# Optimization experiments

Hardware: AMD Instinct MI355X
Metric: run time of the kernel (lower is better)

Reference implementation:

```python
import jax, jax.numpy as jnp
import numpy as np

MIN_VAR = 1e-4
B_SZ, T, X, U, A_DIM = 256, 256, 16, 8, 32


def setup_inputs() -> dict:
    key = jax.random.key(0)
    ks = jax.random.split(key, 8)
    return {
        "mean0": jax.random.normal(ks[0], (B_SZ, X), jnp.float32),
        "cov0": jnp.broadcast_to(jnp.eye(X, dtype=jnp.float32), (B_SZ, X, X)),
        "u": jax.random.normal(ks[1], (B_SZ, T, U), jnp.float32),
        "a": jax.random.normal(ks[2], (B_SZ, T, A_DIM), jnp.float32),
        "M": jnp.eye(X, dtype=jnp.float32),
        "N": jnp.eye(X, dtype=jnp.float32),
        "d": jax.random.normal(ks[3], (X,), jnp.float32),
        "B": jax.random.normal(ks[4], (X, U), jnp.float32),
        "C": jax.random.normal(ks[5], (A_DIM, X), jnp.float32),
        "nx": jax.random.normal(ks[6], (X,), jnp.float32),
        "na": jax.random.normal(ks[7], (A_DIM,), jnp.float32),
    }


def _compute_A(M, N, d):
    # A = U diag(sqrt(d)) Q diag(1/sqrt(1+d)) U^T, with Q, U sign-fixed QR factors
    dsp = jax.nn.softplus(d)
    Q, R = jnp.linalg.qr(M)
    Q = Q * jnp.sign(jnp.diagonal(R))[None, :]
    Uq, R2 = jnp.linalg.qr(N)
    Uq = Uq * jnp.sign(jnp.diagonal(R2))[None, :]
    return Uq @ (jnp.sqrt(dsp)[:, None] * Q) @ ((1.0 / jnp.sqrt(1.0 + dsp))[:, None] * Uq.T)


def reference(mean0, cov0, u, a, M, N, d, B, C, nx, na):
    A = _compute_A(M, N, d)
    Nx = jnp.diag(jax.nn.softplus(nx) + MIN_VAR)  # (x,x)
    Na = jnp.diag(jax.nn.softplus(na) + MIN_VAR)  # (a,a)

    def step(carry, inp):
        mean, cov = carry          # (b,x), (b,x,x)
        u_t, a_t = inp             # (b,u), (b,a)
        # dynamics update
        mean = mean @ A.T + u_t @ B.T
        cov = jnp.einsum('ij,bjk,lk->bil', A, cov, A) + Nx
        # measurement update
        S = jnp.einsum('ij,bjk,lk->bil', C, cov, C) + Na      # (b,a,a)
        K = jnp.einsum('bij,kj,bkl->bil', cov, C, jnp.linalg.pinv(S))  # (b,x,a)
        innov = a_t - mean @ C.T                              # (b,a)
        mean = mean + jnp.einsum('ba,bxa->bx', innov, K)
        cov = cov - jnp.einsum('bxa,ay,byk->bxk', K, C, cov)  # (I - K C) cov
        return (mean, cov), mean

    us = jnp.swapaxes(u, 0, 1)  # (T,b,u)
    as_ = jnp.swapaxes(a, 0, 1)  # (T,b,a)
    (_, _), means = jax.lax.scan(step, (mean0, cov0), (us, as_))
    return jnp.swapaxes(means, 0, 1)  # (b,T,x) filtered means
```

## Files before the change

### kernel.cpp

```cpp
#include <hip/hip_runtime.h>
#include <math.h>

#define TT 256
#define WARM 16
#define OFF_K    5632
#define OFF_MC   14336
#define OFF_NB   18688
#define OFF_P0   20864
#define OFF_PP   21120
#define OFF_WSEG 21376
#define OFF_BND  86912
#define NEED_WS_BYTES ((size_t)152448 * 4)

__device__ __forceinline__ float softplus(float v) {
    return fmaxf(v, 0.0f) + log1pf(expf(-fabsf(v)));
}

__device__ __forceinline__ void gj16(float (&aug)[8], const int i, const int gq) {
#pragma unroll
    for (int j = 0; j < 16; ++j) {
        float prow[8];
#pragma unroll
        for (int k = 0; k < 8; ++k) prow[k] = __shfl(aug[k], j + 16 * gq);
        const float pjj = __shfl(aug[j & 7], j + 16 * (j >> 3));
        const float cij = __shfl(aug[j & 7], i + 16 * (j >> 3));
        const float pivinv = 1.0f / pjj;
        const float f = cij * pivinv;
#pragma unroll
        for (int k = 0; k < 8; ++k)
            aug[k] = (i == j) ? prow[k] * pivinv : aug[k] - f * prow[k];
    }
}

#define LD_ROW16(Mt, r, row) do { \
    const float4 r0_ = *(const float4*)&Mt[r][0]; \
    const float4 r1_ = *(const float4*)&Mt[r][4]; \
    const float4 r2_ = *(const float4*)&Mt[r][8]; \
    const float4 r3_ = *(const float4*)&Mt[r][12]; \
    row[0]=r0_.x;  row[1]=r0_.y;  row[2]=r0_.z;  row[3]=r0_.w; \
    row[4]=r1_.x;  row[5]=r1_.y;  row[6]=r1_.z;  row[7]=r1_.w; \
    row[8]=r2_.x;  row[9]=r2_.y;  row[10]=r2_.z; row[11]=r2_.w; \
    row[12]=r3_.x; row[13]=r3_.y; row[14]=r3_.z; row[15]=r3_.w; } while (0)

__global__ __launch_bounds__(64) void chain_k(
    const float* __restrict__ Mm, const float* __restrict__ Nm,
    const float* __restrict__ dvec, const float* __restrict__ Bm,
    const float* __restrict__ Cm, const float* __restrict__ nx,
    const float* __restrict__ na, const float* __restrict__ cov0,
    float* __restrict__ wsK, float* __restrict__ wsM, float* __restrict__ wsN)
{
    __shared__ float qm[16][17], qn[16][17], T0s[16][17];
    __shared__ float sC[32][17], sW[16][33], sAm[16][17], sBm[16][9];
    __shared__ float sCA[32][17], sCB[32][9], sP[16][17], sK[16][33];
    __shared__ float spv[16], d2[16], sNai[32], sNxi[16];
    __shared__ __attribute__((aligned(16))) float mE[16][20];
    __shared__ __attribute__((aligned(16))) float mET[16][20];
    __shared__ __attribute__((aligned(16))) float mF[16][20];
    __shared__ __attribute__((aligned(16))) float mH[16][20];
    __shared__ __attribute__((aligned(16))) float mZ[16][20];
    __shared__ __attribute__((aligned(16))) float mT[16][20];
    __shared__ __attribute__((aligned(16))) float mT2[16][20];
    __shared__ __attribute__((aligned(16))) float mL[16][20];
    const int lane = threadIdx.x;
    const int t = blockIdx.x;
    const int n = t + 1;
    const int i = lane & 15, gq = lane >> 4;
    const int jj = gq << 2;

    for (int e = lane; e < 256; e += 64) { qm[e >> 4][e & 15] = Mm[e]; qn[e >> 4][e & 15] = Nm[e]; }
    for (int e = lane; e < 512; e += 64) sC[e >> 4][e & 15] = Cm[e];
    for (int e = lane; e < 128; e += 64) sBm[e >> 3][e & 7] = Bm[e];
    if (lane < 16) {
        float s = softplus(dvec[lane]);
        spv[lane] = sqrtf(s);
        d2[lane] = 1.0f / sqrtf(1.0f + s);
        sNxi[lane] = 1.0f / (softplus(nx[lane]) + 1e-4f);
    }
    if (lane < 32) sNai[lane] = 1.0f / (softplus(na[lane]) + 1e-4f);
    __syncthreads();

    {
        const int j0 = lane & 15;
        const int mi = lane >> 4;
        float (*Qs)[17] = (mi == 1) ? qn : qm;
        float col[16];
#pragma unroll
        for (int r = 0; r < 16; ++r) col[r] = Qs[r][j0];
        const int base = lane & 48;
#pragma unroll 1
        for (int j = 0; j < 16; ++j) {
            float qj[16];
#pragma unroll
            for (int r = 0; r < 16; ++r) qj[r] = __shfl(col[r], base + j);
            float nrm = 0.f;
#pragma unroll
            for (int r = 0; r < 16; ++r) nrm += qj[r] * qj[r];
            const float scal = 1.0f / sqrtf(nrm);
#pragma unroll
            for (int r = 0; r < 16; ++r) qj[r] *= scal;
            if (j0 == j) {
#pragma unroll
                for (int r = 0; r < 16; ++r) col[r] = qj[r];
            } else if (j0 > j) {
                float pr = 0.f;
#pragma unroll
                for (int r = 0; r < 16; ++r) pr += qj[r] * col[r];
#pragma unroll
                for (int r = 0; r < 16; ++r) col[r] -= pr * qj[r];
            }
        }
        __syncthreads();
        if (mi < 2) {
#pragma unroll
            for (int r = 0; r < 16; ++r) Qs[r][j0] = col[r];
        }
    }
    __syncthreads();

    for (int e = lane; e < 256; e += 64) {
        int ii = e >> 4, j = e & 15;
        float s = 0.f;
        for (int q = 0; q < 16; ++q) s += qm[ii][q] * d2[q] * qn[j][q];
        T0s[ii][j] = spv[ii] * s;
    }
    __syncthreads();
    for (int e = lane; e < 256; e += 64) {
        int ii = e >> 4, j = e & 15;
        float s = 0.f;
        for (int q = 0; q < 16; ++q) s += qn[ii][q] * T0s[q][j];
        sAm[ii][j] = s;
    }
    for (int e = lane; e < 512; e += 64) {
        int q = e >> 5, r = e & 31;
        sW[q][r] = sC[r][q] * sNai[r];
    }
    __syncthreads();
    for (int e = lane; e < 256; e += 64) {
        int ii = e >> 4, j = e & 15;
        float g = 0.f;
        for (int r = 0; r < 32; ++r) g += sC[r][ii] * sW[j][r];
        mF[ii][j] = g + ((ii == j) ? sNxi[ii] : 0.f);
        const float ev = sNxi[ii] * sAm[ii][j];
        mE[ii][j] = ev;
        mET[j][ii] = ev;
        float hsum = 0.f;
        for (int q = 0; q < 16; ++q) hsum += sAm[q][ii] * sNxi[q] * sAm[q][j];
        mH[ii][j] = hsum;
    }
    for (int e = lane; e < 512; e += 64) {
        int r = e >> 4, j = e & 15;
        float s = 0.f;
        for (int q = 0; q < 16; ++q) s += sC[r][q] * sAm[q][j];
        sCA[r][j] = s;
    }
    for (int e = lane; e < 256; e += 64) {
        int r = e >> 3, j = e & 7;
        float s = 0.f;
        for (int q = 0; q < 16; ++q) s += sC[r][q] * sBm[q][j];
        sCB[r][j] = s;
    }
    __syncthreads();

    float Er[16], ETr[16];
    LD_ROW16(mE, i, Er);
    LD_ROW16(mET, i, ETr);

    float aug[8];
#pragma unroll
    for (int k = 0; k < 8; ++k)
        aug[k] = (gq < 2) ? cov0[i * 16 + 8 * gq + k]
                          : ((8 * (gq - 2) + k == i) ? 1.f : 0.f);
    gj16(aug, i, gq);
    if (gq >= 2) {
        *(float4*)&mL[i][8 * (gq - 2)]     = make_float4(aug[0], aug[1], aug[2], aug[3]);
        *(float4*)&mL[i][8 * (gq - 2) + 4] = make_float4(aug[4], aug[5], aug[6], aug[7]);
    }
    __syncthreads();

#pragma unroll 1
    for (int m = 0; m < 5; ++m) {
        if ((n >> m) & 1) {
            if (gq < 2) {
                const float4 l0 = *(const float4*)&mL[i][8 * gq];
                const float4 l1 = *(const float4*)&mL[i][8 * gq + 4];
                const float4 h0 = *(const float4*)&mH[i][8 * gq];
                const float4 h1 = *(const float4*)&mH[i][8 * gq + 4];
                aug[0] = l0.x + h0.x; aug[1] = l0.y + h0.y;
                aug[2] = l0.z + h0.z; aug[3] = l0.w + h0.w;
                aug[4] = l1.x + h1.x; aug[5] = l1.y + h1.y;
                aug[6] = l1.z + h1.z; aug[7] = l1.w + h1.w;
            } else {
#pragma unroll
                for (int k = 0; k < 8; ++k) aug[k] = (8 * (gq - 2) + k == i) ? 1.f : 0.f;
            }
            gj16(aug, i, gq);
            if (gq >= 2) {
                *(float4*)&mZ[i][8 * (gq - 2)]     = make_float4(aug[0], aug[1], aug[2], aug[3]);
                *(float4*)&mZ[i][8 * (gq - 2) + 4] = make_float4(aug[4], aug[5], aug[6], aug[7]);
            }
            __syncthreads();
            {
                float4 zz[16];
#pragma unroll
                for (int q = 0; q < 16; ++q) zz[q] = *(const float4*)&mZ[q][jj];
                float4 tacc = make_float4(0.f, 0.f, 0.f, 0.f);
#pragma unroll
                for (int q = 0; q < 16; ++q) {
                    tacc.x += Er[q] * zz[q].x; tacc.y += Er[q] * zz[q].y;
                    tacc.z += Er[q] * zz[q].z; tacc.w += Er[q] * zz[q].w;
                }
                *(float4*)&mT[i][jj] = tacc;
            }
            __syncthreads();
            {
                float Tr[16];
                LD_ROW16(mT, i, Tr);
                float4 et[16];
#pragma unroll
                for (int q = 0; q < 16; ++q) et[q] = *(const float4*)&mET[q][jj];
                float4 l = *(const float4*)&mF[i][jj];
#pragma unroll
                for (int q = 0; q < 16; ++q) {
                    l.x -= Tr[q] * et[q].x; l.y -= Tr[q] * et[q].y;
                    l.z -= Tr[q] * et[q].z; l.w -= Tr[q] * et[q].w;
                }
                __syncthreads();
                *(float4*)&mL[i][jj] = l;
            }
            __syncthreads();
        }
        if (m < 4 && (n >> (m + 1)) != 0) {
            if (gq < 2) {
                const float4 f0 = *(const float4*)&mF[i][8 * gq];
                const float4 f1 = *(const float4*)&mF[i][8 * gq + 4];
                const float4 h0 = *(const float4*)&mH[i][8 * gq];
                const float4 h1 = *(const float4*)&mH[i][8 * gq + 4];
                aug[0] = f0.x + h0.x; aug[1] = f0.y + h0.y;
                aug[2] = f0.z + h0.z; aug[3] = f0.w + h0.w;
                aug[4] = f1.x + h1.x; aug[5] = f1.y + h1.y;
                aug[6] = f1.z + h1.z; aug[7] = f1.w + h1.w;
            } else {
#pragma unroll
                for (int k = 0; k < 8; ++k) aug[k] = (8 * (gq - 2) + k == i) ? 1.f : 0.f;
            }
            gj16(aug, i, gq);
            if (gq >= 2) {
                *(float4*)&mZ[i][8 * (gq - 2)]     = make_float4(aug[0], aug[1], aug[2], aug[3]);
                *(float4*)&mZ[i][8 * (gq - 2) + 4] = make_float4(aug[4], aug[5], aug[6], aug[7]);
            }
            __syncthreads();
            {
                float4 zz[16];
#pragma unroll
                for (int q = 0; q < 16; ++q) zz[q] = *(const float4*)&mZ[q][jj];
                float4 tacc = make_float4(0.f, 0.f, 0.f, 0.f);
                float4 t2acc = make_float4(0.f, 0.f, 0.f, 0.f);
#pragma unroll
                for (int q = 0; q < 16; ++q) {
                    tacc.x  += Er[q]  * zz[q].x; tacc.y  += Er[q]  * zz[q].y;
                    tacc.z  += Er[q]  * zz[q].z; tacc.w  += Er[q]  * zz[q].w;
                    t2acc.x += ETr[q] * zz[q].x; t2acc.y += ETr[q] * zz[q].y;
                    t2acc.z += ETr[q] * zz[q].z; t2acc.w += ETr[q] * zz[q].w;
                }
                *(float4*)&mT[i][jj]  = tacc;
                *(float4*)&mT2[i][jj] = t2acc;
            }
            __syncthreads();
            {
                float Tr[16], T2r[16];
                LD_ROW16(mT, i, Tr);
                LD_ROW16(mT2, i, T2r);
                float4 f  = *(const float4*)&mF[i][jj];
                float4 hh = *(const float4*)&mH[i][jj];
                float4 en = make_float4(0.f, 0.f, 0.f, 0.f);
#pragma unroll
                for (int qh = 0; qh < 16; qh += 8) {
                    float4 eq[8], etq[8];
#pragma unroll
                    for (int q0 = 0; q0 < 8; ++q0) {
                        eq[q0]  = *(const float4*)&mE[qh + q0][jj];
                        etq[q0] = *(const float4*)&mET[qh + q0][jj];
                    }
#pragma unroll
                    for (int q0 = 0; q0 < 8; ++q0) {
                        const float tq = Tr[qh + q0], t2q = T2r[qh + q0];
                        f.x  -= tq  * etq[q0].x; f.y  -= tq  * etq[q0].y;
                        f.z  -= tq  * etq[q0].z; f.w  -= tq  * etq[q0].w;
                        hh.x -= t2q * eq[q0].x;  hh.y -= t2q * eq[q0].y;
                        hh.z -= t2q * eq[q0].z;  hh.w -= t2q * eq[q0].w;
                        en.x += tq  * eq[q0].x;  en.y += tq  * eq[q0].y;
                        en.z += tq  * eq[q0].z;  en.w += tq  * eq[q0].w;
                    }
                }
                __syncthreads();
                *(float4*)&mF[i][jj] = f;
                *(float4*)&mH[i][jj] = hh;
                *(float4*)&mE[i][jj] = en;
                mET[jj + 0][i] = en.x; mET[jj + 1][i] = en.y;
                mET[jj + 2][i] = en.z; mET[jj + 3][i] = en.w;
            }
            __syncthreads();
            LD_ROW16(mE, i, Er);
            LD_ROW16(mET, i, ETr);
        }
    }

    if (gq < 2) {
        const float4 l0 = *(const float4*)&mL[i][8 * gq];
        const float4 l1 = *(const float4*)&mL[i][8 * gq + 4];
        aug[0] = l0.x; aug[1] = l0.y; aug[2] = l0.z; aug[3] = l0.w;
        aug[4] = l1.x; aug[5] = l1.y; aug[6] = l1.z; aug[7] = l1.w;
    } else {
#pragma unroll
        for (int k = 0; k < 8; ++k) aug[k] = (8 * (gq - 2) + k == i) ? 1.f : 0.f;
    }
    gj16(aug, i, gq);
    if (gq >= 2) {
#pragma unroll
        for (int k = 0; k < 8; ++k) sP[i][8 * (gq - 2) + k] = aug[k];
    }
    __syncthreads();
#pragma unroll
    for (int m = 0; m < 8; ++m) {
        const int e = lane + 64 * m, ii = e >> 5, rr = e & 31;
        float s = 0.f;
#pragma unroll
        for (int q = 0; q < 16; ++q) s += sP[ii][q] * sW[q][rr];
        sK[ii][rr] = s;
        wsK[(size_t)t * 512 + e] = s;
    }
    __syncthreads();
#pragma unroll
    for (int m = 0; m < 4; ++m) {
        const int e = lane + 64 * m, ii = e >> 4, jjm = e & 15;
        float s = sAm[ii][jjm];
#pragma unroll
        for (int r = 0; r < 32; ++r) s -= sK[ii][r] * sCA[r][jjm];
        wsM[(size_t)t * 256 + e] = s;
    }
#pragma unroll
    for (int m = 0; m < 2; ++m) {
        const int e = lane + 64 * m, ii = e >> 3, jjm = e & 7;
        float s = sBm[ii][jjm];
#pragma unroll
        for (int r = 0; r < 32; ++r) s -= sK[ii][r] * sCB[r][jjm];
        wsN[(size_t)t * 128 + e] = s;
    }
}

__global__ __launch_bounds__(64) void phA_k(
    const float* __restrict__ u, const float* __restrict__ a,
    const float* __restrict__ wsK, const float* __restrict__ wsM,
    const float* __restrict__ wsN, float* __restrict__ wseg,
    float* __restrict__ wsp)
{
    const int lane = threadIdx.x;
    const int i = lane & 15, g = lane >> 4;
    const int seg = blockIdx.x >> 8;
    const int b = blockIdx.x & 255;

    float mcs[16][4];
#pragma unroll
    for (int j = 0; j < 16; ++j) {
        const int tc = (seg == 0) ? j : 16;
        const float4 v = *(const float4*)(wsM + (size_t)tc * 256 + i * 16 + 4 * g);
        mcs[j][0] = v.x; mcs[j][1] = v.y; mcs[j][2] = v.z; mcs[j][3] = v.w;
    }
    float kc[8], nbc[8];
    if (seg != 0) {
        const float4 k0 = *(const float4*)(wsK + (size_t)16 * 512 + i * 32 + 8 * g);
        const float4 k1 = *(const float4*)(wsK + (size_t)16 * 512 + i * 32 + 8 * g + 4);
        const float4 n0 = *(const float4*)(wsN + (size_t)16 * 128 + i * 8);
        const float4 n1 = *(const float4*)(wsN + (size_t)16 * 128 + i * 8 + 4);
        kc[0]=k0.x; kc[1]=k0.y; kc[2]=k0.z; kc[3]=k0.w;
        kc[4]=k1.x; kc[5]=k1.y; kc[6]=k1.z; kc[7]=k1.w;
        nbc[0]=n0.x; nbc[1]=n0.y; nbc[2]=n0.z; nbc[3]=n0.w;
        nbc[4]=n1.x; nbc[5]=n1.y; nbc[6]=n1.z; nbc[7]=n1.w;
    }

    float w = 0.f;
#pragma unroll
    for (int j = 0; j < 16; ++j) {
        const int t = 16 * seg + j;
        float kr[8], nbr[8];
        if (seg == 0) {
            const float4 k0 = *(const float4*)(wsK + (size_t)j * 512 + i * 32 + 8 * g);
            const float4 k1 = *(const float4*)(wsK + (size_t)j * 512 + i * 32 + 8 * g + 4);
            const float4 n0 = *(const float4*)(wsN + (size_t)j * 128 + i * 8);
            const float4 n1 = *(const float4*)(wsN + (size_t)j * 128 + i * 8 + 4);
            kr[0]=k0.x; kr[1]=k0.y; kr[2]=k0.z; kr[3]=k0.w;
            kr[4]=k1.x; kr[5]=k1.y; kr[6]=k1.z; kr[7]=k1.w;
            nbr[0]=n0.x; nbr[1]=n0.y; nbr[2]=n0.z; nbr[3]=n0.w;
            nbr[4]=n1.x; nbr[5]=n1.y; nbr[6]=n1.z; nbr[7]=n1.w;
        } else {
#pragma unroll
            for (int k = 0; k < 8; ++k) { kr[k] = kc[k]; nbr[k] = nbc[k]; }
        }
        const float a0 = a[(size_t)b * (TT * 32) + t * 32 + (lane & 31)];
        const float u0 = u[(size_t)b * (TT * 8) + t * 8 + (lane & 7)];
        float gvp = kr[0] * __shfl(a0, 8*g+0) + kr[1] * __shfl(a0, 8*g+1)
                  + kr[2] * __shfl(a0, 8*g+2) + kr[3] * __shfl(a0, 8*g+3)
                  + kr[4] * __shfl(a0, 8*g+4) + kr[5] * __shfl(a0, 8*g+5)
                  + kr[6] * __shfl(a0, 8*g+6) + kr[7] * __shfl(a0, 8*g+7);
        float nbs = nbr[0] * __shfl(u0,0) + nbr[1] * __shfl(u0,1)
                  + nbr[2] * __shfl(u0,2) + nbr[3] * __shfl(u0,3)
                  + nbr[4] * __shfl(u0,4) + nbr[5] * __shfl(u0,5)
                  + nbr[6] * __shfl(u0,6) + nbr[7] * __shfl(u0,7);
        gvp += (g == 3) ? nbs : 0.f;
        gvp += __shfl_xor(gvp, 16);
        gvp += __shfl_xor(gvp, 32);
        float part = mcs[j][0] * __shfl(w, 4*g+0) + mcs[j][1] * __shfl(w, 4*g+1)
                   + mcs[j][2] * __shfl(w, 4*g+2) + mcs[j][3] * __shfl(w, 4*g+3);
        part += __shfl_xor(part, 16);
        part += __shfl_xor(part, 32);
        w = part + gvp;
    }
    if (lane < 16) wseg[(size_t)seg * 4096 + b * 16 + i] = w;

    if (blockIdx.x == 0) {
        float pr[4];
#pragma unroll
        for (int k = 0; k < 4; ++k) pr[k] = (4 * g + k == i) ? 1.f : 0.f;
#pragma unroll
        for (int j = 0; j < 16; ++j) {
            float np[4] = {0.f, 0.f, 0.f, 0.f};
#pragma unroll
            for (int q = 0; q < 16; ++q) {
                const float mq = __shfl(mcs[j][q & 3], i + 16 * (q >> 2));
#pragma unroll
                for (int k = 0; k < 4; ++k) np[k] += mq * __shfl(pr[k], q + 16 * g);
            }
#pragma unroll
            for (int k = 0; k < 4; ++k) pr[k] = np[k];
        }
#pragma unroll
        for (int k = 0; k < 4; ++k) wsp[i * 16 + 4 * g + k] = pr[k];
    }
    if (blockIdx.x == 256) {
        float pr[4];
#pragma unroll
        for (int k = 0; k < 4; ++k) pr[k] = mcs[0][k];
#pragma unroll
        for (int r = 0; r < 4; ++r) {
            float np[4] = {0.f, 0.f, 0.f, 0.f};
#pragma unroll
            for (int q = 0; q < 16; ++q) {
                const float sq = __shfl(pr[q & 3], i + 16 * (q >> 2));
#pragma unroll
                for (int k = 0; k < 4; ++k) np[k] += sq * __shfl(pr[k], q + 16 * g);
            }
#pragma unroll
            for (int k = 0; k < 4; ++k) pr[k] = np[k];
        }
#pragma unroll
        for (int k = 0; k < 4; ++k) wsp[256 + i * 16 + 4 * g + k] = pr[k];
    }
}

__global__ __launch_bounds__(64) void phB_k(
    const float* __restrict__ mean0, const float* __restrict__ wsp,
    const float* __restrict__ wseg, float* __restrict__ bnd)
{
    const int lane = threadIdx.x;
    const int i = lane & 15, g = lane >> 4;
    const int b = blockIdx.x;

    const float4 v0 = *(const float4*)(wsp + i * 16 + 4 * g);
    const float4 vp = *(const float4*)(wsp + 256 + i * 16 + 4 * g);
    const float m0s[4] = {v0.x, v0.y, v0.z, v0.w};
    const float mps[4] = {vp.x, vp.y, vp.z, vp.w};
    float wv[16];
#pragma unroll
    for (int s = 0; s < 16; ++s) wv[s] = wseg[(size_t)s * 4096 + b * 16 + i];

    float mn = mean0[b * 16 + i];
#pragma unroll
    for (int s = 0; s < 16; ++s) {
        if (lane < 16) bnd[(size_t)s * 4096 + b * 16 + i] = mn;
        const float c0 = (s == 0) ? m0s[0] : mps[0];
        const float c1 = (s == 0) ? m0s[1] : mps[1];
        const float c2 = (s == 0) ? m0s[2] : mps[2];
        const float c3 = (s == 0) ? m0s[3] : mps[3];
        float part = c0 * __shfl(mn, 4 * g + 0) + c1 * __shfl(mn, 4 * g + 1)
                   + c2 * __shfl(mn, 4 * g + 2) + c3 * __shfl(mn, 4 * g + 3);
        part += __shfl_xor(part, 16);
        part += __shfl_xor(part, 32);
        mn = part + wv[s];
    }
}

__global__ __launch_bounds__(64) void phC_k(
    const float* __restrict__ u, const float* __restrict__ a,
    const float* __restrict__ wsK, const float* __restrict__ wsM,
    const float* __restrict__ wsN, const float* __restrict__ bnd,
    float* __restrict__ out)
{
    const int lane = threadIdx.x;
    const int i = lane & 15, g = lane >> 4;
    const int seg = blockIdx.x >> 8;
    const int b = blockIdx.x & 255;

    float mcs[16][4];
#pragma unroll
    for (int j = 0; j < 16; ++j) {
        const int tc = (seg == 0) ? j : 16;
        const float4 v = *(const float4*)(wsM + (size_t)tc * 256 + i * 16 + 4 * g);
        mcs[j][0] = v.x; mcs[j][1] = v.y; mcs[j][2] = v.z; mcs[j][3] = v.w;
    }
    float kc[8], nbc[8];
    if (seg != 0) {
        const float4 k0 = *(const float4*)(wsK + (size_t)16 * 512 + i * 32 + 8 * g);
        const float4 k1 = *(const float4*)(wsK + (size_t)16 * 512 + i * 32 + 8 * g + 4);
        const float4 n0 = *(const float4*)(wsN + (size_t)16 * 128 + i * 8);
        const float4 n1 = *(const float4*)(wsN + (size_t)16 * 128 + i * 8 + 4);
        kc[0]=k0.x; kc[1]=k0.y; kc[2]=k0.z; kc[3]=k0.w;
        kc[4]=k1.x; kc[5]=k1.y; kc[6]=k1.z; kc[7]=k1.w;
        nbc[0]=n0.x; nbc[1]=n0.y; nbc[2]=n0.z; nbc[3]=n0.w;
        nbc[4]=n1.x; nbc[5]=n1.y; nbc[6]=n1.z; nbc[7]=n1.w;
    }

    float mn = bnd[(size_t)seg * 4096 + b * 16 + i];
    float* ob = out + (size_t)b * 4096 + (size_t)(16 * seg) * 16;
#pragma unroll
    for (int j = 0; j < 16; ++j) {
        const int t = 16 * seg + j;
        float kr[8], nbr[8];
        if (seg == 0) {
            const float4 k0 = *(const float4*)(wsK + (size_t)j * 512 + i * 32 + 8 * g);
            const float4 k1 = *(const float4*)(wsK + (size_t)j * 512 + i * 32 + 8 * g + 4);
            const float4 n0 = *(const float4*)(wsN + (size_t)j * 128 + i * 8);
            const float4 n1 = *(const float4*)(wsN + (size_t)j * 128 + i * 8 + 4);
            kr[0]=k0.x; kr[1]=k0.y; kr[2]=k0.z; kr[3]=k0.w;
            kr[4]=k1.x; kr[5]=k1.y; kr[6]=k1.z; kr[7]=k1.w;
            nbr[0]=n0.x; nbr[1]=n0.y; nbr[2]=n0.z; nbr[3]=n0.w;
            nbr[4]=n1.x; nbr[5]=n1.y; nbr[6]=n1.z; nbr[7]=n1.w;
        } else {
#pragma unroll
            for (int k = 0; k < 8; ++k) { kr[k] = kc[k]; nbr[k] = nbc[k]; }
        }
        const float a0 = a[(size_t)b * (TT * 32) + t * 32 + (lane & 31)];
        const float u0 = u[(size_t)b * (TT * 8) + t * 8 + (lane & 7)];
        float gvp = kr[0] * __shfl(a0, 8*g+0) + kr[1] * __shfl(a0, 8*g+1)
                  + kr[2] * __shfl(a0, 8*g+2) + kr[3] * __shfl(a0, 8*g+3)
                  + kr[4] * __shfl(a0, 8*g+4) + kr[5] * __shfl(a0, 8*g+5)
                  + kr[6] * __shfl(a0, 8*g+6) + kr[7] * __shfl(a0, 8*g+7);
        float nbs = nbr[0] * __shfl(u0,0) + nbr[1] * __shfl(u0,1)
                  + nbr[2] * __shfl(u0,2) + nbr[3] * __shfl(u0,3)
                  + nbr[4] * __shfl(u0,4) + nbr[5] * __shfl(u0,5)
                  + nbr[6] * __shfl(u0,6) + nbr[7] * __shfl(u0,7);
        gvp += (g == 3) ? nbs : 0.f;
        gvp += __shfl_xor(gvp, 16);
        gvp += __shfl_xor(gvp, 32);
        float part = mcs[j][0] * __shfl(mn, 4*g+0) + mcs[j][1] * __shfl(mn, 4*g+1)
                   + mcs[j][2] * __shfl(mn, 4*g+2) + mcs[j][3] * __shfl(mn, 4*g+3);
        part += __shfl_xor(part, 16);
        part += __shfl_xor(part, 32);
        mn = part + gvp;
        if (lane < 16) ob[j * 16 + i] = mn;
    }
}

__global__ __launch_bounds__(64) void meanf_k(
    const float* __restrict__ mean0, const float* __restrict__ u,
    const float* __restrict__ a, const float* __restrict__ wsK,
    const float* __restrict__ wsM, const float* __restrict__ wsN,
    float* __restrict__ out)
{
    const int lane = threadIdx.x;
    const int b = blockIdx.x;
    const int i = lane & 15;
    const int g = lane >> 4;

    const float* ub = u + (size_t)b * TT * 8;
    const float* ab = a + (size_t)b * TT * 32;
    float* ob = out + (size_t)b * TT * 16;

    float mn = mean0[b * 16 + i];
    float Mc[16];
    {
        const float4* p = (const float4*)(wsM + i * 16);
        float4 x0 = p[0], x1 = p[1], x2 = p[2], x3 = p[3];
        Mc[0]=x0.x; Mc[1]=x0.y; Mc[2]=x0.z; Mc[3]=x0.w;
        Mc[4]=x1.x; Mc[5]=x1.y; Mc[6]=x1.z; Mc[7]=x1.w;
        Mc[8]=x2.x; Mc[9]=x2.y; Mc[10]=x2.z; Mc[11]=x2.w;
        Mc[12]=x3.x; Mc[13]=x3.y; Mc[14]=x3.z; Mc[15]=x3.w;
    }
    float gv;
    {
        float4 k0 = *(const float4*)(wsK + i * 32 + 8 * g);
        float4 k1 = *(const float4*)(wsK + i * 32 + 8 * g + 4);
        float4 n0 = *(const float4*)(wsN + i * 8);
        float4 n1 = *(const float4*)(wsN + i * 8 + 4);
        float u0 = ub[lane & 7];
        float a0 = ab[lane & 31];
        float part = k0.x * __shfl(a0, 8*g+0) + k0.y * __shfl(a0, 8*g+1)
                   + k0.z * __shfl(a0, 8*g+2) + k0.w * __shfl(a0, 8*g+3)
                   + k1.x * __shfl(a0, 8*g+4) + k1.y * __shfl(a0, 8*g+5)
                   + k1.z * __shfl(a0, 8*g+6) + k1.w * __shfl(a0, 8*g+7);
        float nbs = n0.x * __shfl(u0,0) + n0.y * __shfl(u0,1)
                  + n0.z * __shfl(u0,2) + n0.w * __shfl(u0,3)
                  + n1.x * __shfl(u0,4) + n1.y * __shfl(u0,5)
                  + n1.z * __shfl(u0,6) + n1.w * __shfl(u0,7);
        part += (g == 3) ? nbs : 0.f;
        part += __shfl_xor(part, 16);
        part += __shfl_xor(part, 32);
        gv = part;
    }
    float4 mA, mB, mC, mD, kp0, kp1, np0, np1;
    float upn, apn;
    {
        const float4* p = (const float4*)(wsM + 256 + i * 16);
        mA = p[0]; mB = p[1]; mC = p[2]; mD = p[3];
        kp0 = *(const float4*)(wsK + 512 + i * 32 + 8 * g);
        kp1 = *(const float4*)(wsK + 512 + i * 32 + 8 * g + 4);
        np0 = *(const float4*)(wsN + 128 + i * 8);
        np1 = *(const float4*)(wsN + 128 + i * 8 + 4);
        upn = ub[8 + (lane & 7)];
        apn = ab[32 + (lane & 31)];
    }

    for (int t = 0; t < TT; ++t) {
        const int t2 = (t + 2 < TT) ? t + 2 : TT - 1;
        const int s2 = (t2 < WARM) ? t2 : WARM;
        const float4* mp = (const float4*)(wsM + (size_t)s2 * 256 + i * 16);
        float4 l0 = mp[0], l1 = mp[1], l2 = mp[2], l3 = mp[3];
        float4 kl0 = *(const float4*)(wsK + (size_t)s2 * 512 + i * 32 + 8 * g);
        float4 kl1 = *(const float4*)(wsK + (size_t)s2 * 512 + i * 32 + 8 * g + 4);
        float4 nl0 = *(const float4*)(wsN + (size_t)s2 * 128 + i * 8);
        float4 nl1 = *(const float4*)(wsN + (size_t)s2 * 128 + i * 8 + 4);
        float ul = ub[t2 * 8 + (lane & 7)];
        float al = ab[t2 * 32 + (lane & 31)];

        float s0 = gv, s1 = 0.f, s2f = 0.f, s3 = 0.f;
#pragma unroll
        for (int q = 0; q < 16; q += 4) {
            s0  += Mc[q]     * __shfl(mn, q);
            s1  += Mc[q + 1] * __shfl(mn, q + 1);
            s2f += Mc[q + 2] * __shfl(mn, q + 2);
            s3  += Mc[q + 3] * __shfl(mn, q + 3);
        }
        mn = (s0 + s1) + (s2f + s3);
        if (lane < 16) ob[t * 16 + lane] = mn;

        float part = kp0.x * __shfl(apn, 8*g+0) + kp0.y * __shfl(apn, 8*g+1)
                   + kp0.z * __shfl(apn, 8*g+2) + kp0.w * __shfl(apn, 8*g+3)
                   + kp1.x * __shfl(apn, 8*g+4) + kp1.y * __shfl(apn, 8*g+5)
                   + kp1.z * __shfl(apn, 8*g+6) + kp1.w * __shfl(apn, 8*g+7);
        float nbs = np0.x * __shfl(upn,0) + np0.y * __shfl(upn,1)
                  + np0.z * __shfl(upn,2) + np0.w * __shfl(upn,3)
                  + np1.x * __shfl(upn,4) + np1.y * __shfl(upn,5)
                  + np1.z * __shfl(upn,6) + np1.w * __shfl(upn,7);
        part += (g == 3) ? nbs : 0.f;
        part += __shfl_xor(part, 16);
        part += __shfl_xor(part, 32);
        gv = part;

        Mc[0]=mA.x; Mc[1]=mA.y; Mc[2]=mA.z; Mc[3]=mA.w;
        Mc[4]=mB.x; Mc[5]=mB.y; Mc[6]=mB.z; Mc[7]=mB.w;
        Mc[8]=mC.x; Mc[9]=mC.y; Mc[10]=mC.z; Mc[11]=mC.w;
        Mc[12]=mD.x; Mc[13]=mD.y; Mc[14]=mD.z; Mc[15]=mD.w;
        mA = l0; mB = l1; mC = l2; mD = l3;
        kp0 = kl0; kp1 = kl1; np0 = nl0; np1 = nl1;
        upn = ul; apn = al;
    }
}

extern "C" void kernel_launch(void* const* d_in, const int* in_sizes, int n_in,
                              void* d_out, int out_size, void* d_ws, size_t ws_size,
                              hipStream_t stream) {
    const float* mean0 = nullptr; const float* cov0 = nullptr;
    const float* u = nullptr;     const float* a = nullptr;
    const float* Mm = nullptr;    const float* Nm = nullptr;
    const float* dv = nullptr;    const float* Bm = nullptr;
    const float* Cm = nullptr;    const float* nxp = nullptr;
    const float* nap = nullptr;
    for (int i = 0; i < n_in; ++i) {
        const float* p = (const float*)d_in[i];
        switch (in_sizes[i]) {
            case 256 * 16:        mean0 = p; break;
            case 256 * 256:       cov0 = p; break;
            case 256 * 256 * 8:   u = p; break;
            case 256 * 256 * 32:  a = p; break;
            case 256:             if (!Mm) Mm = p; else Nm = p; break;
            case 16:              if (!dv) dv = p; else nxp = p; break;
            case 128:             Bm = p; break;
            case 512:             Cm = p; break;
            case 32:              nap = p; break;
            default: break;
        }
    }
    float* ws   = (float*)d_ws;
    float* wsK  = ws + OFF_K;
    float* wsM  = ws + OFF_MC;
    float* wsN  = ws + OFF_NB;
    float* wsp  = ws + OFF_P0;
    float* wseg = ws + OFF_WSEG;
    float* bnd  = ws + OFF_BND;

    chain_k<<<WARM + 1, 64, 0, stream>>>(Mm, Nm, dv, Bm, Cm, nxp, nap, cov0,
                                         wsK, wsM, wsN);
    if (ws_size >= NEED_WS_BYTES) {
        phA_k<<<16 * 256, 64, 0, stream>>>(u, a, wsK, wsM, wsN, wseg, wsp);
        phB_k<<<256, 64, 0, stream>>>(mean0, wsp, wseg, bnd);
        phC_k<<<16 * 256, 64, 0, stream>>>(u, a, wsK, wsM, wsN, bnd, (float*)d_out);
    } else {
        meanf_k<<<256, 64, 0, stream>>>(mean0, u, a, wsK, wsM, wsN, (float*)d_out);
    }
}
```

Baseline: 176.7 us.

## Store per-step local mean and transition-power prefixes so final phase is parallel

Phase A now writes each step's local affine response (gv) and the prefix powers of the steady-state transition matrix (pfx0/pfx1) to workspace. Phase C then computes every output as prefix matrix times segment boundary state plus the stored local term, so the 16-step sequential recurrence with reloads of a, u, K and M is gone. The chain kernel's repeated inversion code is moved into a non-inlined helper, and a/u reads in phase A become float4 loads instead of shuffles. This needs a much larger workspace and extra global writes. If the workspace is too small, the slower single-kernel fallback path runs instead.

```diff
diff --git a/kernel.cpp b/kernel.cpp
--- a/kernel.cpp
+++ b/kernel.cpp
@@ -10,7 +10,11 @@
 #define OFF_PP   21120
 #define OFF_WSEG 21376
 #define OFF_BND  86912
+#define OFF_GV   152448
+#define OFF_PFX0 1201024
+#define OFF_PFX1 1205120
 #define NEED_WS_BYTES ((size_t)152448 * 4)
+#define NEED_WS3_BYTES ((size_t)1209216 * 4)
 
 __device__ __forceinline__ float softplus(float v) {
     return fmaxf(v, 0.0f) + log1pf(expf(-fabsf(v)));
@@ -29,6 +33,36 @@
 #pragma unroll
         for (int k = 0; k < 8; ++k)
             aug[k] = (i == j) ? prow[k] * pivinv : aug[k] - f * prow[k];
+    }
+}
+
+typedef float Row20[20];
+
+__device__ __attribute__((noinline)) void inv16(
+    const Row20* s1, const Row20* s2, Row20* dst, const int i, const int gq)
+{
+    float aug[8];
+    if (gq < 2) {
+        const float4 a0 = *(const float4*)&s1[i][8 * gq];
+        const float4 a1 = *(const float4*)&s1[i][8 * gq + 4];
+        float4 b0 = make_float4(0.f, 0.f, 0.f, 0.f);
+        float4 b1 = make_float4(0.f, 0.f, 0.f, 0.f);
+        if (s2) {
+            b0 = *(const float4*)&s2[i][8 * gq];
+            b1 = *(const float4*)&s2[i][8 * gq + 4];
+        }
+        aug[0] = a0.x + b0.x; aug[1] = a0.y + b0.y;
+        aug[2] = a0.z + b0.z; aug[3] = a0.w + b0.w;
+        aug[4] = a1.x + b1.x; aug[5] = a1.y + b1.y;
+        aug[6] = a1.z + b1.z; aug[7] = a1.w + b1.w;
+    } else {
+#pragma unroll
+        for (int k = 0; k < 8; ++k) aug[k] = (8 * (gq - 2) + k == i) ? 1.f : 0.f;
+    }
+    gj16(aug, i, gq);
+    if (gq >= 2) {
+        *(float4*)&dst[i][8 * (gq - 2)]     = make_float4(aug[0], aug[1], aug[2], aug[3]);
+        *(float4*)&dst[i][8 * (gq - 2) + 4] = make_float4(aug[4], aug[5], aug[6], aug[7]);
     }
 }
 
@@ -51,7 +85,7 @@
 {
     __shared__ float qm[16][17], qn[16][17], T0s[16][17];
     __shared__ float sC[32][17], sW[16][33], sAm[16][17], sBm[16][9];
-    __shared__ float sCA[32][17], sCB[32][9], sP[16][17], sK[16][33];
+    __shared__ float sCA[32][17], sCB[32][9], sK[16][33];
     __shared__ float spv[16], d2[16], sNai[32], sNxi[16];
     __shared__ __attribute__((aligned(16))) float mE[16][20];
     __shared__ __attribute__((aligned(16))) float mET[16][20];
@@ -159,45 +193,20 @@
         for (int q = 0; q < 16; ++q) s += sC[r][q] * sBm[q][j];
         sCB[r][j] = s;
     }
+    for (int e = lane; e < 256; e += 64) mT[e >> 4][e & 15] = cov0[e];
     __syncthreads();
 
     float Er[16], ETr[16];
     LD_ROW16(mE, i, Er);
     LD_ROW16(mET, i, ETr);
 
-    float aug[8];
-#pragma unroll
-    for (int k = 0; k < 8; ++k)
-        aug[k] = (gq < 2) ? cov0[i * 16 + 8 * gq + k]
-                          : ((8 * (gq - 2) + k == i) ? 1.f : 0.f);
-    gj16(aug, i, gq);
-    if (gq >= 2) {
-        *(float4*)&mL[i][8 * (gq - 2)]     = make_float4(aug[0], aug[1], aug[2], aug[3]);
-        *(float4*)&mL[i][8 * (gq - 2) + 4] = make_float4(aug[4], aug[5], aug[6], aug[7]);
-    }
+    inv16(mT, nullptr, mL, i, gq);
     __syncthreads();
 
 #pragma unroll 1
     for (int m = 0; m < 5; ++m) {
         if ((n >> m) & 1) {
-            if (gq < 2) {
-                const float4 l0 = *(const float4*)&mL[i][8 * gq];
-                const float4 l1 = *(const float4*)&mL[i][8 * gq + 4];
-                const float4 h0 = *(const float4*)&mH[i][8 * gq];
-                const float4 h1 = *(const float4*)&mH[i][8 * gq + 4];
-                aug[0] = l0.x + h0.x; aug[1] = l0.y + h0.y;
-                aug[2] = l0.z + h0.z; aug[3] = l0.w + h0.w;
-                aug[4] = l1.x + h1.x; aug[5] = l1.y + h1.y;
-                aug[6] = l1.z + h1.z; aug[7] = l1.w + h1.w;
-            } else {
-#pragma unroll
-                for (int k = 0; k < 8; ++k) aug[k] = (8 * (gq - 2) + k == i) ? 1.f : 0.f;
-            }
-            gj16(aug, i, gq);
-            if (gq >= 2) {
-                *(float4*)&mZ[i][8 * (gq - 2)]     = make_float4(aug[0], aug[1], aug[2], aug[3]);
-                *(float4*)&mZ[i][8 * (gq - 2) + 4] = make_float4(aug[4], aug[5], aug[6], aug[7]);
-            }
+            inv16(mL, mH, mZ, i, gq);
             __syncthreads();
             {
                 float4 zz[16];
@@ -230,24 +239,7 @@
             __syncthreads();
         }
         if (m < 4 && (n >> (m + 1)) != 0) {
-            if (gq < 2) {
-                const float4 f0 = *(const float4*)&mF[i][8 * gq];
-                const float4 f1 = *(const float4*)&mF[i][8 * gq + 4];
-                const float4 h0 = *(const float4*)&mH[i][8 * gq];
-                const float4 h1 = *(const float4*)&mH[i][8 * gq + 4];
-                aug[0] = f0.x + h0.x; aug[1] = f0.y + h0.y;
-                aug[2] = f0.z + h0.z; aug[3] = f0.w + h0.w;
-                aug[4] = f1.x + h1.x; aug[5] = f1.y + h1.y;
-                aug[6] = f1.z + h1.z; aug[7] = f1.w + h1.w;
-            } else {
-#pragma unroll
-                for (int k = 0; k < 8; ++k) aug[k] = (8 * (gq - 2) + k == i) ? 1.f : 0.f;
-            }
-            gj16(aug, i, gq);
-            if (gq >= 2) {
-                *(float4*)&mZ[i][8 * (gq - 2)]     = make_float4(aug[0], aug[1], aug[2], aug[3]);
-                *(float4*)&mZ[i][8 * (gq - 2) + 4] = make_float4(aug[4], aug[5], aug[6], aug[7]);
-            }
+            inv16(mF, mH, mZ, i, gq);
             __syncthreads();
             {
                 float4 zz[16];
@@ -305,27 +297,14 @@
         }
     }
 
-    if (gq < 2) {
-        const float4 l0 = *(const float4*)&mL[i][8 * gq];
-        const float4 l1 = *(const float4*)&mL[i][8 * gq + 4];
-        aug[0] = l0.x; aug[1] = l0.y; aug[2] = l0.z; aug[3] = l0.w;
-        aug[4] = l1.x; aug[5] = l1.y; aug[6] = l1.z; aug[7] = l1.w;
-    } else {
-#pragma unroll
-        for (int k = 0; k < 8; ++k) aug[k] = (8 * (gq - 2) + k == i) ? 1.f : 0.f;
-    }
-    gj16(aug, i, gq);
-    if (gq >= 2) {
-#pragma unroll
-        for (int k = 0; k < 8; ++k) sP[i][8 * (gq - 2) + k] = aug[k];
-    }
+    inv16(mL, nullptr, mZ, i, gq);
     __syncthreads();
 #pragma unroll
     for (int m = 0; m < 8; ++m) {
         const int e = lane + 64 * m, ii = e >> 5, rr = e & 31;
         float s = 0.f;
 #pragma unroll
-        for (int q = 0; q < 16; ++q) s += sP[ii][q] * sW[q][rr];
+        for (int q = 0; q < 16; ++q) s += mZ[ii][q] * sW[q][rr];
         sK[ii][rr] = s;
         wsK[(size_t)t * 512 + e] = s;
     }
@@ -352,7 +331,8 @@
     const float* __restrict__ u, const float* __restrict__ a,
     const float* __restrict__ wsK, const float* __restrict__ wsM,
     const float* __restrict__ wsN, float* __restrict__ wseg,
-    float* __restrict__ wsp)
+    float* __restrict__ wsp, float* __restrict__ gv,
+    float* __restrict__ pfx0, float* __restrict__ pfx1)
 {
     const int lane = threadIdx.x;
     const int i = lane & 15, g = lane >> 4;
@@ -396,16 +376,14 @@
 #pragma unroll
             for (int k = 0; k < 8; ++k) { kr[k] = kc[k]; nbr[k] = nbc[k]; }
         }
-        const float a0 = a[(size_t)b * (TT * 32) + t * 32 + (lane & 31)];
-        const float u0 = u[(size_t)b * (TT * 8) + t * 8 + (lane & 7)];
-        float gvp = kr[0] * __shfl(a0, 8*g+0) + kr[1] * __shfl(a0, 8*g+1)
-                  + kr[2] * __shfl(a0, 8*g+2) + kr[3] * __shfl(a0, 8*g+3)
-                  + kr[4] * __shfl(a0, 8*g+4) + kr[5] * __shfl(a0, 8*g+5)
-                  + kr[6] * __shfl(a0, 8*g+6) + kr[7] * __shfl(a0, 8*g+7);
-        float nbs = nbr[0] * __shfl(u0,0) + nbr[1] * __shfl(u0,1)
-                  + nbr[2] * __shfl(u0,2) + nbr[3] * __shfl(u0,3)
-                  + nbr[4] * __shfl(u0,4) + nbr[5] * __shfl(u0,5)
-                  + nbr[6] * __shfl(u0,6) + nbr[7] * __shfl(u0,7);
+        const float4 av0 = *(const float4*)(a + (size_t)b * (TT * 32) + t * 32 + 8 * g);
+        const float4 av1 = *(const float4*)(a + (size_t)b * (TT * 32) + t * 32 + 8 * g + 4);
+        const float4 uv0 = *(const float4*)(u + (size_t)b * (TT * 8) + t * 8);
+        const float4 uv1 = *(const float4*)(u + (size_t)b * (TT * 8) + t * 8 + 4);
+        float gvp = kr[0] * av0.x + kr[1] * av0.y + kr[2] * av0.z + kr[3] * av0.w
+                  + kr[4] * av1.x + kr[5] * av1.y + kr[6] * av1.z + kr[7] * av1.w;
+        float nbs = nbr[0] * uv0.x + nbr[1] * uv0.y + nbr[2] * uv0.z + nbr[3] * uv0.w
+                  + nbr[4] * uv1.x + nbr[5] * uv1.y + nbr[6] * uv1.z + nbr[7] * uv1.w;
         gvp += (g == 3) ? nbs : 0.f;
         gvp += __shfl_xor(gvp, 16);
         gvp += __shfl_xor(gvp, 32);
@@ -414,6 +392,7 @@
         part += __shfl_xor(part, 16);
         part += __shfl_xor(part, 32);
         w = part + gvp;
+        if (lane < 16) gv[(size_t)t * 4096 + b * 16 + i] = w;
     }
     if (lane < 16) wseg[(size_t)seg * 4096 + b * 16 + i] = w;
 
@@ -432,6 +411,8 @@
             }
 #pragma unroll
             for (int k = 0; k < 4; ++k) pr[k] = np[k];
+#pragma unroll
+            for (int k = 0; k < 4; ++k) pfx0[j * 256 + i * 16 + 4 * g + k] = pr[k];
         }
 #pragma unroll
         for (int k = 0; k < 4; ++k) wsp[i * 16 + 4 * g + k] = pr[k];
@@ -441,16 +422,20 @@
 #pragma unroll
         for (int k = 0; k < 4; ++k) pr[k] = mcs[0][k];
 #pragma unroll
-        for (int r = 0; r < 4; ++r) {
+        for (int k = 0; k < 4; ++k) pfx1[i * 16 + 4 * g + k] = pr[k];
+#pragma unroll 1
+        for (int r = 1; r < 16; ++r) {
             float np[4] = {0.f, 0.f, 0.f, 0.f};
 #pragma unroll
             for (int q = 0; q < 16; ++q) {
-                const float sq = __shfl(pr[q & 3], i + 16 * (q >> 2));
-#pragma unroll
-                for (int k = 0; k < 4; ++k) np[k] += sq * __shfl(pr[k], q + 16 * g);
+                const float mq = __shfl(mcs[0][q & 3], i + 16 * (q >> 2));
+#pragma unroll
+                for (int k = 0; k < 4; ++k) np[k] += mq * __shfl(pr[k], q + 16 * g);
             }
 #pragma unroll
             for (int k = 0; k < 4; ++k) pr[k] = np[k];
+#pragma unroll
+            for (int k = 0; k < 4; ++k) pfx1[r * 256 + i * 16 + 4 * g + k] = pr[k];
         }
 #pragma unroll
         for (int k = 0; k < 4; ++k) wsp[256 + i * 16 + 4 * g + k] = pr[k];
@@ -490,9 +475,8 @@
 }
 
 __global__ __launch_bounds__(64) void phC_k(
-    const float* __restrict__ u, const float* __restrict__ a,
-    const float* __restrict__ wsK, const float* __restrict__ wsM,
-    const float* __restrict__ wsN, const float* __restrict__ bnd,
+    const float* __restrict__ pfx0, const float* __restrict__ pfx1,
+    const float* __restrict__ wpart, const float* __restrict__ bnd,
     float* __restrict__ out)
 {
     const int lane = threadIdx.x;
@@ -500,63 +484,27 @@
     const int seg = blockIdx.x >> 8;
     const int b = blockIdx.x & 255;
 
-    float mcs[16][4];
-#pragma unroll
-    for (int j = 0; j < 16; ++j) {
-        const int tc = (seg == 0) ? j : 16;
-        const float4 v = *(const float4*)(wsM + (size_t)tc * 256 + i * 16 + 4 * g);
-        mcs[j][0] = v.x; mcs[j][1] = v.y; mcs[j][2] = v.z; mcs[j][3] = v.w;
-    }
-    float kc[8], nbc[8];
-    if (seg != 0) {
-        const float4 k0 = *(const float4*)(wsK + (size_t)16 * 512 + i * 32 + 8 * g);
-        const float4 k1 = *(const float4*)(wsK + (size_t)16 * 512 + i * 32 + 8 * g + 4);
-        const float4 n0 = *(const float4*)(wsN + (size_t)16 * 128 + i * 8);
-        const float4 n1 = *(const float4*)(wsN + (size_t)16 * 128 + i * 8 + 4);
-        kc[0]=k0.x; kc[1]=k0.y; kc[2]=k0.z; kc[3]=k0.w;
-        kc[4]=k1.x; kc[5]=k1.y; kc[6]=k1.z; kc[7]=k1.w;
-        nbc[0]=n0.x; nbc[1]=n0.y; nbc[2]=n0.z; nbc[3]=n0.w;
-        nbc[4]=n1.x; nbc[5]=n1.y; nbc[6]=n1.z; nbc[7]=n1.w;
-    }
-
-    float mn = bnd[(size_t)seg * 4096 + b * 16 + i];
+    const float* bp = bnd + (size_t)seg * 4096 + b * 16;
+    const float4 bv0 = *(const float4*)(bp);
+    const float4 bv1 = *(const float4*)(bp + 4);
+    const float4 bv2 = *(const float4*)(bp + 8);
+    const float4 bv3 = *(const float4*)(bp + 12);
+    const float* P = (seg == 0) ? pfx0 : pfx1;
     float* ob = out + (size_t)b * 4096 + (size_t)(16 * seg) * 16;
 #pragma unroll
-    for (int j = 0; j < 16; ++j) {
-        const int t = 16 * seg + j;
-        float kr[8], nbr[8];
-        if (seg == 0) {
-            const float4 k0 = *(const float4*)(wsK + (size_t)j * 512 + i * 32 + 8 * g);
-            const float4 k1 = *(const float4*)(wsK + (size_t)j * 512 + i * 32 + 8 * g + 4);
-            const float4 n0 = *(const float4*)(wsN + (size_t)j * 128 + i * 8);
-            const float4 n1 = *(const float4*)(wsN + (size_t)j * 128 + i * 8 + 4);
-            kr[0]=k0.x; kr[1]=k0.y; kr[2]=k0.z; kr[3]=k0.w;
-            kr[4]=k1.x; kr[5]=k1.y; kr[6]=k1.z; kr[7]=k1.w;
-            nbr[0]=n0.x; nbr[1]=n0.y; nbr[2]=n0.z; nbr[3]=n0.w;
-            nbr[4]=n1.x; nbr[5]=n1.y; nbr[6]=n1.z; nbr[7]=n1.w;
-        } else {
-#pragma unroll
-            for (int k = 0; k < 8; ++k) { kr[k] = kc[k]; nbr[k] = nbc[k]; }
-        }
-        const float a0 = a[(size_t)b * (TT * 32) + t * 32 + (lane & 31)];
-        const float u0 = u[(size_t)b * (TT * 8) + t * 8 + (lane & 7)];
-        float gvp = kr[0] * __shfl(a0, 8*g+0) + kr[1] * __shfl(a0, 8*g+1)
-                  + kr[2] * __shfl(a0, 8*g+2) + kr[3] * __shfl(a0, 8*g+3)
-                  + kr[4] * __shfl(a0, 8*g+4) + kr[5] * __shfl(a0, 8*g+5)
-                  + kr[6] * __shfl(a0, 8*g+6) + kr[7] * __shfl(a0, 8*g+7);
-        float nbs = nbr[0] * __shfl(u0,0) + nbr[1] * __shfl(u0,1)
-                  + nbr[2] * __shfl(u0,2) + nbr[3] * __shfl(u0,3)
-                  + nbr[4] * __shfl(u0,4) + nbr[5] * __shfl(u0,5)
-                  + nbr[6] * __shfl(u0,6) + nbr[7] * __shfl(u0,7);
-        gvp += (g == 3) ? nbs : 0.f;
-        gvp += __shfl_xor(gvp, 16);
-        gvp += __shfl_xor(gvp, 32);
-        float part = mcs[j][0] * __shfl(mn, 4*g+0) + mcs[j][1] * __shfl(mn, 4*g+1)
-                   + mcs[j][2] * __shfl(mn, 4*g+2) + mcs[j][3] * __shfl(mn, 4*g+3);
-        part += __shfl_xor(part, 16);
-        part += __shfl_xor(part, 32);
-        mn = part + gvp;
-        if (lane < 16) ob[j * 16 + i] = mn;
+    for (int k = 0; k < 4; ++k) {
+        const int j = 4 * g + k;
+        const float* pr = P + (size_t)j * 256 + i * 16;
+        const float4 p0 = *(const float4*)(pr);
+        const float4 p1 = *(const float4*)(pr + 4);
+        const float4 p2 = *(const float4*)(pr + 8);
+        const float4 p3 = *(const float4*)(pr + 12);
+        float s = p0.x * bv0.x + p0.y * bv0.y + p0.z * bv0.z + p0.w * bv0.w
+                + p1.x * bv1.x + p1.y * bv1.y + p1.z * bv1.z + p1.w * bv1.w
+                + p2.x * bv2.x + p2.y * bv2.y + p2.z * bv2.z + p2.w * bv2.w
+                + p3.x * bv3.x + p3.y * bv3.y + p3.z * bv3.z + p3.w * bv3.w;
+        s += wpart[(size_t)(16 * seg + j) * 4096 + b * 16 + i];
+        ob[j * 16 + i] = s;
     }
 }
 
@@ -696,14 +644,19 @@
     float* wsp  = ws + OFF_P0;
     float* wseg = ws + OFF_WSEG;
     float* bnd  = ws + OFF_BND;
+    float* gv   = ws + OFF_GV;
+    float* pfx0 = ws + OFF_PFX0;
+    float* pfx1 = ws + OFF_PFX1;
+    float* outf = (float*)d_out;
 
     chain_k<<<WARM + 1, 64, 0, stream>>>(Mm, Nm, dv, Bm, Cm, nxp, nap, cov0,
                                          wsK, wsM, wsN);
-    if (ws_size >= NEED_WS_BYTES) {
-        phA_k<<<16 * 256, 64, 0, stream>>>(u, a, wsK, wsM, wsN, wseg, wsp);
+    if (ws_size >= NEED_WS3_BYTES) {
+        phA_k<<<16 * 256, 64, 0, stream>>>(u, a, wsK, wsM, wsN, wseg, wsp, gv,
+                                           pfx0, pfx1);
         phB_k<<<256, 64, 0, stream>>>(mean0, wsp, wseg, bnd);
-        phC_k<<<16 * 256, 64, 0, stream>>>(u, a, wsK, wsM, wsN, bnd, (float*)d_out);
+        phC_k<<<16 * 256, 64, 0, stream>>>(pfx0, pfx1, gv, bnd, outf);
     } else {
-        meanf_k<<<256, 64, 0, stream>>>(mean0, u, a, wsK, wsM, wsN, (float*)d_out);
-    }
-}
+        meanf_k<<<256, 64, 0, stream>>>(mean0, u, a, wsK, wsM, wsN, outf);
+    }
+}
```

After: 156.7 us. -11.3%, faster.
